# Kernel tuning notes

Hardware: AMD Instinct MI355X
Metric: run time of the kernel (lower is better)

Reference implementation:

```python
import jax, jax.numpy as jnp
import numpy as np

D_MODEL = 1024
NHEAD = 16
D_K = D_MODEL // NHEAD
MAX_REL = 1024


def setup_inputs() -> dict:
    key = jax.random.key(0)
    ks = jax.random.split(key, 6)
    B, S = 4, 2048
    s = 1.0 / np.sqrt(D_MODEL)
    x = jax.random.normal(ks[0], (B, S, D_MODEL), dtype=jnp.float32)
    W_qkv = jax.random.normal(ks[1], (D_MODEL, 3 * D_MODEL), dtype=jnp.float32) * s
    b_qkv = jnp.zeros((3 * D_MODEL,), dtype=jnp.float32)
    W_out = jax.random.normal(ks[2], (D_MODEL, D_MODEL), dtype=jnp.float32) * s
    b_out = jnp.zeros((D_MODEL,), dtype=jnp.float32)
    # torch init is zeros; use small random so bias path is exercised
    rel_bias = jax.random.normal(ks[3], (2 * MAX_REL + 1, NHEAD), dtype=jnp.float32) * 0.02
    return {"x": x, "W_qkv": W_qkv, "b_qkv": b_qkv, "W_out": W_out,
            "b_out": b_out, "rel_bias": rel_bias}


def reference(x, W_qkv, b_qkv, W_out, b_out, rel_bias):
    B, S, D = x.shape
    qkv = x @ W_qkv + b_qkv                      # [B,S,3D]
    qkv = qkv.reshape(B, S, 3, NHEAD, D_K)
    q, k, v = qkv[:, :, 0], qkv[:, :, 1], qkv[:, :, 2]  # [B,S,H,dk]
    # scores: [B,H,S,S]
    scores = jnp.einsum('bihd,bjhd->bhij', q, k) / jnp.sqrt(jnp.float32(D_K))
    idxs = jnp.arange(S)
    rel = jnp.clip(idxs[:, None] - idxs[None, :] + MAX_REL, 0, 2 * MAX_REL)  # [S,S]
    bias = rel_bias[rel]                         # [S,S,H]
    scores = scores + jnp.transpose(bias, (2, 0, 1))[None]  # broadcast over batch
    attn = jax.nn.softmax(scores, axis=-1)       # dropout p=0 (eval)
    out = jnp.einsum('bhij,bjhd->bihd', attn, v).reshape(B, S, D)
    return out @ W_out + b_out
```

## Files before the change

### kernel.cpp

```cpp
#include <hip/hip_runtime.h>

#define S_LEN 2048
#define NHEADS 16
#define DK 64
#define DMODEL 1024
#define QSCALE 0.18033688011f

typedef float f32x4 __attribute__((ext_vector_type(4)));
typedef _Float16 f16x8 __attribute__((ext_vector_type(8)));
typedef _Float16 f16x4 __attribute__((ext_vector_type(4)));
typedef __fp16 h16x2 __attribute__((ext_vector_type(2)));

__device__ __forceinline__ unsigned short f2h_bits(float f) {
  _Float16 h = (_Float16)f;
  unsigned short u; __builtin_memcpy(&u, &h, 2); return u;
}

__device__ __forceinline__ f32x4 mfma16(f16x8 a, f16x8 b, f32x4 c) {
  return __builtin_amdgcn_mfma_f32_16x16x32_f16(a, b, c, 0, 0, 0);
}
__device__ __forceinline__ f32x4 mfma16k16(f16x4 a, f16x4 b, f32x4 c) {
  return __builtin_amdgcn_mfma_f32_16x16x16f16(a, b, c, 0, 0, 0);
}
__device__ __forceinline__ f16x8 frag_ld(const unsigned short* p) {
  return *(const f16x8*)p;
}

#define GLD_LDS(g, l)                                                          \
  __builtin_amdgcn_global_load_lds(                                            \
      (const __attribute__((address_space(1))) void*)(g),                      \
      (__attribute__((address_space(3))) void*)(l), 16, 0, 0)

__global__ void convert_f32_f16(const float* __restrict__ in,
                                unsigned short* __restrict__ out, int n4) {
  int i = blockIdx.x * blockDim.x + threadIdx.x;
  if (i < n4) {
    f32x4 v = *(const f32x4*)(in + (size_t)i * 4);
    unsigned short o[4];
#pragma unroll
    for (int j = 0; j < 4; j++) o[j] = f2h_bits(v[j]);
    *(uint2*)(out + (size_t)i * 4) = *(const uint2*)o;
  }
}

__global__ void transpose_f32_f16(const float* __restrict__ in,
                                  unsigned short* __restrict__ out, int R, int C) {
  __shared__ unsigned short tile[32][33];
  int bx = blockIdx.x * 32, by = blockIdx.y * 32;
  int tx = threadIdx.x, ty = threadIdx.y;
  for (int i = ty; i < 32; i += 8)
    tile[i][tx] = f2h_bits(in[(size_t)(by + i) * C + bx + tx]);
  __syncthreads();
  for (int i = ty; i < 32; i += 8)
    out[(size_t)(bx + i) * R + by + tx] = tile[tx][i];
}

__launch_bounds__(256)
__global__ void gemm_bt(const unsigned short* __restrict__ A,
                        const unsigned short* __restrict__ Bt,
                        int M, int N, int K, int mode,
                        const float* __restrict__ bias,
                        float* __restrict__ out0,
                        unsigned short* __restrict__ q_o,
                        unsigned short* __restrict__ k_o,
                        unsigned short* __restrict__ v_o) {
  __shared__ __attribute__((aligned(16))) unsigned short As[128 * 32];
  __shared__ __attribute__((aligned(16))) unsigned short Bs[128 * 32];
  const int tid = threadIdx.x;
  const int w = tid >> 6, lane = tid & 63;
  const int wm = w >> 1, wn = w & 1;
  const int col = lane & 15, quad = lane >> 4;
  const int m0 = blockIdx.y * 128, n0 = blockIdx.x * 128;
  const f32x4 fzero = {0.f, 0.f, 0.f, 0.f};
  f32x4 acc[4][4];
#pragma unroll
  for (int i = 0; i < 4; i++)
#pragma unroll
    for (int j = 0; j < 4; j++) acc[i][j] = fzero;

  for (int k0 = 0; k0 < K; k0 += 32) {
    __syncthreads();
#pragma unroll
    for (int it = 0; it < 2; it++) {
      int c = it * 256 + tid;
      GLD_LDS(A + (size_t)(m0 + (c >> 2)) * K + k0 + (c & 3) * 8, &As[c * 8]);
      GLD_LDS(Bt + (size_t)(n0 + (c >> 2)) * K + k0 + (c & 3) * 8, &Bs[c * 8]);
    }
    __syncthreads();
    f16x8 af[4], bfr[4];
#pragma unroll
    for (int mi = 0; mi < 4; mi++)
      af[mi] = frag_ld(&As[(wm * 64 + mi * 16 + col) * 32 + quad * 8]);
#pragma unroll
    for (int ni = 0; ni < 4; ni++)
      bfr[ni] = frag_ld(&Bs[(wn * 64 + ni * 16 + col) * 32 + quad * 8]);
#pragma unroll
    for (int mi = 0; mi < 4; mi++)
#pragma unroll
      for (int ni = 0; ni < 4; ni++)
        acc[mi][ni] = mfma16(af[mi], bfr[ni], acc[mi][ni]);
  }

#pragma unroll
  for (int mi = 0; mi < 4; mi++) {
#pragma unroll
    for (int ni = 0; ni < 4; ni++) {
      int gm_b = m0 + wm * 64 + mi * 16 + quad * 4;
      int gn = n0 + wn * 64 + ni * 16 + col;
      float bv = bias[gn];
#pragma unroll
      for (int r = 0; r < 4; r++) {
        int gm = gm_b + r;
        float val = acc[mi][ni][r] + bv;
        if (mode == 1) {
          out0[(size_t)gm * N + gn] = val;
        } else {
          int b = gm >> 11, s = gm & 2047;
          int t = gn >> 10, hd = gn & 1023;
          int h = hd >> 6, d = hd & 63;
          size_t bh = (size_t)(b * NHEADS + h);
          if (t == 0) {
            q_o[(bh * S_LEN + s) * DK + d] = f2h_bits(val * QSCALE);
          } else if (t == 1) {
            k_o[(bh * S_LEN + s) * DK + d] = f2h_bits(val);
          } else {
            v_o[(bh * DK + d) * S_LEN + s] = f2h_bits(val);
          }
        }
      }
    }
  }
}

__launch_bounds__(256)
__global__ void attn_kernel(const unsigned short* __restrict__ Q,
                            const unsigned short* __restrict__ K,
                            const unsigned short* __restrict__ Vt,
                            const float* __restrict__ rel_bias,
                            unsigned short* __restrict__ ctx) {
  __shared__ __attribute__((aligned(16))) unsigned short Ks[64 * 64];
  __shared__ __attribute__((aligned(16))) unsigned short Vs[64 * 64];
  __shared__ float brev[4096];
  const int tid = threadIdx.x;
  const int w = tid >> 6, lane = tid & 63;
  const int col = lane & 15, quad = lane >> 4;
  const int c7 = col & 7;
  const int bid = blockIdx.x;
  const int qt = bid & 31, bh = bid >> 5;
  const int h = bh & (NHEADS - 1), b = bh >> 4;
  const unsigned short* qp = Q + (size_t)bh * S_LEN * DK;
  const unsigned short* kp = K + (size_t)bh * S_LEN * DK;
  const unsigned short* vp = Vt + (size_t)bh * DK * S_LEN;
  const f32x4 fzero = {0.f, 0.f, 0.f, 0.f};
  const f16x4 ones = {(_Float16)1.f, (_Float16)1.f, (_Float16)1.f, (_Float16)1.f};

#pragma unroll
  for (int it = 0; it < 16; it++) {
    int t = it * 256 + tid;
    int rel = 3072 - t;
    rel = rel < 0 ? 0 : (rel > 2048 ? 2048 : rel);
    brev[t] = rel_bias[rel * NHEADS + h] * 1.44269504089f;
  }

  const int row_base = qt * 64 + w * 16;
  f16x8 qa0 = frag_ld(qp + (size_t)(row_base + col) * DK + quad * 8);
  f16x8 qa1 = frag_ld(qp + (size_t)(row_base + col) * DK + 32 + quad * 8);

  const int tq = quad * 4 - (row_base + col) + 2048;

  f32x4 o[4];
  f32x4 lacc;
#pragma unroll
  for (int ni = 0; ni < 4; ni++) o[ni] = fzero;
  lacc = fzero;

  for (int ck = 0; ck < S_LEN / 64; ck++) {
    const int j0 = ck * 64;
    __syncthreads();
#pragma unroll
    for (int it = 0; it < 2; it++) {
      int c = it * 256 + tid;
      int row = c >> 3, gs = c & 7, g = gs ^ (row & 7);
      GLD_LDS(kp + (size_t)(j0 + row) * DK + g * 8, &Ks[c * 8]);
      GLD_LDS(vp + (size_t)row * S_LEN + j0 + g * 8, &Vs[c * 8]);
    }
    __syncthreads();

    const float* bp = &brev[j0 + tq];
    f32x4 sc4[4];
#pragma unroll
    for (int ni = 0; ni < 4; ni++) {
      f32x4 bias4;
#pragma unroll
      for (int r = 0; r < 4; r++) bias4[r] = bp[ni * 16 + r];
      f16x8 kb0 = frag_ld(&Ks[(ni * 16 + col) * 64 + (quad ^ c7) * 8]);
      f16x8 kb1 = frag_ld(&Ks[(ni * 16 + col) * 64 + ((quad | 4) ^ c7) * 8]);
      sc4[ni] = mfma16(kb1, qa1, mfma16(kb0, qa0, bias4));
    }
    f16x4 pa[4];
#pragma unroll
    for (int ni = 0; ni < 4; ni++) {
      float p0 = __builtin_amdgcn_exp2f(sc4[ni][0]);
      float p1 = __builtin_amdgcn_exp2f(sc4[ni][1]);
      float p2 = __builtin_amdgcn_exp2f(sc4[ni][2]);
      float p3 = __builtin_amdgcn_exp2f(sc4[ni][3]);
      h16x2 lo = __builtin_amdgcn_cvt_pkrtz(p0, p1);
      h16x2 hi = __builtin_amdgcn_cvt_pkrtz(p2, p3);
      f16x4 t;
      __builtin_memcpy(&t, &lo, 4);
      __builtin_memcpy(((char*)&t) + 4, &hi, 4);
      pa[ni] = t;
    }
#pragma unroll
    for (int ni_d = 0; ni_d < 4; ni_d++) {
#pragma unroll
      for (int ni_k = 0; ni_k < 4; ni_k++) {
        int g = ni_k * 2 + (quad >> 1);
        f16x4 vb = *(const f16x4*)&Vs[(ni_d * 16 + col) * 64 + (g ^ c7) * 8 + (quad & 1) * 4];
        o[ni_d] = mfma16k16(pa[ni_k], vb, o[ni_d]);
      }
    }
#pragma unroll
    for (int ni_k = 0; ni_k < 4; ni_k++)
      lacc = mfma16k16(pa[ni_k], ones, lacc);
  }
  float inv_r[4];
#pragma unroll
  for (int r = 0; r < 4; r++) inv_r[r] = 1.0f / lacc[r];
#pragma unroll
  for (int r = 0; r < 4; r++) {
    int srow = row_base + quad * 4 + r;
#pragma unroll
    for (int ni = 0; ni < 4; ni++) {
      int d = ni * 16 + col;
      ctx[((size_t)b * S_LEN + srow) * DMODEL + h * DK + d] = f2h_bits(o[ni][r] * inv_r[r]);
    }
  }
}

extern "C" void kernel_launch(void* const* d_in, const int* in_sizes, int n_in,
                              void* d_out, int out_size, void* d_ws, size_t ws_size,
                              hipStream_t stream) {
  (void)in_sizes; (void)n_in; (void)out_size; (void)ws_size;
  const float* x        = (const float*)d_in[0];
  const float* W_qkv    = (const float*)d_in[1];
  const float* b_qkv    = (const float*)d_in[2];
  const float* W_out    = (const float*)d_in[3];
  const float* b_out    = (const float*)d_in[4];
  const float* rel_bias = (const float*)d_in[5];
  float* out = (float*)d_out;

  char* ws = (char*)d_ws;
  unsigned short* xh     = (unsigned short*)(ws + 0);
  unsigned short* ctxh   = (unsigned short*)(ws + 0);
  unsigned short* Wqkv_t = (unsigned short*)(ws + 16777216);
  unsigned short* Wout_t = (unsigned short*)(ws + 23068672);
  unsigned short* Qb     = (unsigned short*)(ws + 25165824);
  unsigned short* Kb     = (unsigned short*)(ws + 41943040);
  unsigned short* Vtb    = (unsigned short*)(ws + 58720256);

  convert_f32_f16<<<(8192 * 1024 / 4 + 255) / 256, 256, 0, stream>>>(x, xh, 8192 * 1024 / 4);
  transpose_f32_f16<<<dim3(3072 / 32, 1024 / 32), dim3(32, 8), 0, stream>>>(W_qkv, Wqkv_t, 1024, 3072);
  transpose_f32_f16<<<dim3(1024 / 32, 1024 / 32), dim3(32, 8), 0, stream>>>(W_out, Wout_t, 1024, 1024);
  gemm_bt<<<dim3(3072 / 128, 8192 / 128), 256, 0, stream>>>(
      xh, Wqkv_t, 8192, 3072, 1024, 0, b_qkv, nullptr, Qb, Kb, Vtb);
  attn_kernel<<<4 * NHEADS * (S_LEN / 64), 256, 0, stream>>>(Qb, Kb, Vtb, rel_bias, ctxh);
  gemm_bt<<<dim3(1024 / 128, 8192 / 128), 256, 0, stream>>>(
      ctxh, Wout_t, 8192, 1024, 1024, 1, b_out, out, nullptr, nullptr, nullptr);
}
```

Baseline: 351.4 us.

## Double-buffer K/V tiles in attention, remap blocks per XCD, vectorize V epilogue

The attention kernel now keeps two K/V shared-memory buffers. The next 64-key tile is issued into the spare buffer right after the single per-iteration barrier, so global-to-LDS loads overlap the current tile's MFMA and exp work, and the second barrier per iteration goes away. Block indices are remapped so blocks for the same batch-head land on the same XCD slot pattern, aiming for better L2 reuse of K/V. The QKV GEMM epilogue hoists the index math out of the row loop and writes the transposed V output as one 8-byte store instead of four scalar stores. Doubling the K/V buffers raises LDS use and may affect occupancy.

```diff
diff --git a/kernel.cpp b/kernel.cpp
--- a/kernel.cpp
+++ b/kernel.cpp
@@ -108,24 +108,26 @@
       int gm_b = m0 + wm * 64 + mi * 16 + quad * 4;
       int gn = n0 + wn * 64 + ni * 16 + col;
       float bv = bias[gn];
-#pragma unroll
-      for (int r = 0; r < 4; r++) {
-        int gm = gm_b + r;
-        float val = acc[mi][ni][r] + bv;
-        if (mode == 1) {
-          out0[(size_t)gm * N + gn] = val;
+      if (mode == 1) {
+#pragma unroll
+        for (int r = 0; r < 4; r++)
+          out0[(size_t)(gm_b + r) * N + gn] = acc[mi][ni][r] + bv;
+      } else {
+        int b = gm_b >> 11, s0 = gm_b & 2047;
+        int t = gn >> 10, hd = gn & 1023;
+        int h = hd >> 6, d = hd & 63;
+        size_t bh = (size_t)(b * NHEADS + h);
+        if (t == 2) {
+          unsigned short o4[4];
+#pragma unroll
+          for (int r = 0; r < 4; r++) o4[r] = f2h_bits(acc[mi][ni][r] + bv);
+          *(uint2*)&v_o[(bh * DK + d) * S_LEN + s0] = *(const uint2*)o4;
         } else {
-          int b = gm >> 11, s = gm & 2047;
-          int t = gn >> 10, hd = gn & 1023;
-          int h = hd >> 6, d = hd & 63;
-          size_t bh = (size_t)(b * NHEADS + h);
-          if (t == 0) {
-            q_o[(bh * S_LEN + s) * DK + d] = f2h_bits(val * QSCALE);
-          } else if (t == 1) {
-            k_o[(bh * S_LEN + s) * DK + d] = f2h_bits(val);
-          } else {
-            v_o[(bh * DK + d) * S_LEN + s] = f2h_bits(val);
-          }
+          unsigned short* dst = (t == 0) ? q_o : k_o;
+          float sc = (t == 0) ? QSCALE : 1.0f;
+#pragma unroll
+          for (int r = 0; r < 4; r++)
+            dst[(bh * S_LEN + s0 + r) * DK + d] = f2h_bits((acc[mi][ni][r] + bv) * sc);
         }
       }
     }
@@ -138,15 +140,17 @@
                             const unsigned short* __restrict__ Vt,
                             const float* __restrict__ rel_bias,
                             unsigned short* __restrict__ ctx) {
-  __shared__ __attribute__((aligned(16))) unsigned short Ks[64 * 64];
-  __shared__ __attribute__((aligned(16))) unsigned short Vs[64 * 64];
+  __shared__ __attribute__((aligned(16))) unsigned short Ks[2][64 * 64];
+  __shared__ __attribute__((aligned(16))) unsigned short Vs[2][64 * 64];
   __shared__ float brev[4096];
   const int tid = threadIdx.x;
   const int w = tid >> 6, lane = tid & 63;
   const int col = lane & 15, quad = lane >> 4;
   const int c7 = col & 7;
   const int bid = blockIdx.x;
-  const int qt = bid & 31, bh = bid >> 5;
+  const int xcd = bid & 7, slot = bid >> 3;
+  const int bh = (slot >> 5) * 8 + xcd;
+  const int qt = slot & 31;
   const int h = bh & (NHEADS - 1), b = bh >> 4;
   const unsigned short* qp = Q + (size_t)bh * S_LEN * DK;
   const unsigned short* kp = K + (size_t)bh * S_LEN * DK;
@@ -169,22 +173,27 @@
   const int tq = quad * 4 - (row_base + col) + 2048;
 
   f32x4 o[4];
-  f32x4 lacc;
+  f32x4 lacc = fzero;
 #pragma unroll
   for (int ni = 0; ni < 4; ni++) o[ni] = fzero;
-  lacc = fzero;
-
-  for (int ck = 0; ck < S_LEN / 64; ck++) {
-    const int j0 = ck * 64;
-    __syncthreads();
+
+  auto stage = [&](int bi, int jj) {
 #pragma unroll
     for (int it = 0; it < 2; it++) {
       int c = it * 256 + tid;
       int row = c >> 3, gs = c & 7, g = gs ^ (row & 7);
-      GLD_LDS(kp + (size_t)(j0 + row) * DK + g * 8, &Ks[c * 8]);
-      GLD_LDS(vp + (size_t)row * S_LEN + j0 + g * 8, &Vs[c * 8]);
-    }
+      GLD_LDS(kp + (size_t)(jj + row) * DK + g * 8, &Ks[bi][c * 8]);
+      GLD_LDS(vp + (size_t)row * S_LEN + jj + g * 8, &Vs[bi][c * 8]);
+    }
+  };
+
+  stage(0, 0);
+
+  for (int ck = 0; ck < S_LEN / 64; ck++) {
+    const int j0 = ck * 64;
+    const int cur = ck & 1;
     __syncthreads();
+    if (ck < S_LEN / 64 - 1) stage(cur ^ 1, j0 + 64);
 
     const float* bp = &brev[j0 + tq];
     f32x4 sc4[4];
@@ -193,8 +202,8 @@
       f32x4 bias4;
 #pragma unroll
       for (int r = 0; r < 4; r++) bias4[r] = bp[ni * 16 + r];
-      f16x8 kb0 = frag_ld(&Ks[(ni * 16 + col) * 64 + (quad ^ c7) * 8]);
-      f16x8 kb1 = frag_ld(&Ks[(ni * 16 + col) * 64 + ((quad | 4) ^ c7) * 8]);
+      f16x8 kb0 = frag_ld(&Ks[cur][(ni * 16 + col) * 64 + (quad ^ c7) * 8]);
+      f16x8 kb1 = frag_ld(&Ks[cur][(ni * 16 + col) * 64 + ((quad | 4) ^ c7) * 8]);
       sc4[ni] = mfma16(kb1, qa1, mfma16(kb0, qa0, bias4));
     }
     f16x4 pa[4];
@@ -216,7 +225,7 @@
 #pragma unroll
       for (int ni_k = 0; ni_k < 4; ni_k++) {
         int g = ni_k * 2 + (quad >> 1);
-        f16x4 vb = *(const f16x4*)&Vs[(ni_d * 16 + col) * 64 + (g ^ c7) * 8 + (quad & 1) * 4];
+        f16x4 vb = *(const f16x4*)&Vs[cur][(ni_d * 16 + col) * 64 + (g ^ c7) * 8 + (quad & 1) * 4];
         o[ni_d] = mfma16k16(pa[ni_k], vb, o[ni_d]);
       }
     }
```

After: 342.0 us. 1.03x faster.
